# Optimization experiments

Measured on AMD Instinct MI355X. Metric: run time of the kernel, lower is better.

## Reference

```python
import jax, jax.numpy as jnp
import numpy as np

RADIUS = 50
HEADS = 4
BN_EPS = 1e-5


def setup_inputs() -> dict:
    key = jax.random.key(0)
    B, C, L = 2, 256, 1536
    D = C // HEADS
    ks = jax.random.split(key, 8)
    s = 0.05  # weight init scale
    return {
        "x": jax.random.normal(ks[0], (B, C, L), jnp.float32),
        "Wc": jax.random.normal(ks[1], (C, C), jnp.float32) * s,
        "bc": jnp.zeros((C,), jnp.float32),
        "Wq": jax.random.normal(ks[2], (C, C), jnp.float32) * s,
        "bq": jnp.zeros((C,), jnp.float32),
        "Wk": jax.random.normal(ks[3], (C, C), jnp.float32) * s,
        "bk": jnp.zeros((C,), jnp.float32),
        "emb": jax.random.normal(ks[4], (2 * RADIUS + 1, D), jnp.float32) * s,
        "Wf": jax.random.normal(ks[5], (C, C), jnp.float32) * s,
        "bf": jnp.zeros((C,), jnp.float32),
        "gamma": jnp.ones((C,), jnp.float32),
        "beta": jnp.zeros((C,), jnp.float32),
        "scale": jnp.full((C,), 0.1, jnp.float32),
    }


def reference(x, Wc, bc, Wq, bq, Wk, bk, emb, Wf, bf, gamma, beta, scale):
    B, C, L = x.shape
    H = HEADS
    D = C // H
    R = RADIUS

    def conv1x1(W, b, y):  # 1x1 Conv1d == per-position matmul
        return jnp.einsum('oc,bcl->bol', W, y) + b[None, :, None]

    def split(y):  # [B,C,L] -> [B,H,D,L]
        return y.reshape(B, H, D, L)

    content = split(conv1x1(Wc, bc, x))
    query = split(conv1x1(Wq, bq, x))
    key_ = split(conv1x1(Wk, bk, x))

    steps = jnp.arange(L)
    relative = steps[:, None] - steps[None, :]                 # [L,L]
    rel_clamped = jnp.clip(relative, -R, R)
    embs = emb[R + rel_clamped]                                # [L,L,D] gather

    dots = jnp.einsum('bhct,bhcs->bhts', query, key_)          # [B,H,L,L]
    dots = dots + 0.3 * jnp.einsum('bhct,tsc->bhts', query, embs)
    dots = jnp.where(jnp.abs(relative) <= R, dots, -jnp.inf)   # band mask

    weights = jax.nn.softmax(dots, axis=-1)                    # [B,H,L,L]

    out = jnp.einsum('bhts,bhcs->bhct', weights, content)      # [B,H,D,L]
    out = out + 0.3 * jnp.einsum('bhts,tsc->bhct', weights, embs)
    out = out.reshape(B, C, L)

    out = conv1x1(Wf, bf, out)
    # BatchNorm1d in training mode: batch stats over (B, L) per channel
    mean = out.mean(axis=(0, 2), keepdims=True)
    var = out.var(axis=(0, 2), keepdims=True)
    out = (out - mean) / jnp.sqrt(var + BN_EPS)
    out = out * gamma[None, :, None] + beta[None, :, None]
    return jax.nn.relu(out) * scale[None, :, None]
```

## Files before the change

kernel.cpp:

```cpp
#include <hip/hip_runtime.h>

typedef unsigned short u16;
typedef unsigned int u32;
typedef __bf16 bf16x8 __attribute__((ext_vector_type(8)));
typedef float f32x4 __attribute__((ext_vector_type(4)));

#define MFMA16 __builtin_amdgcn_mfma_f32_16x16x32_bf16

__device__ __forceinline__ u16 f2bf(float f) {
    u32 u = __float_as_uint(f);
    u32 r = (u + 0x7fffu + ((u >> 16) & 1u)) >> 16;
    return (u16)r;
}
__device__ __forceinline__ float bf2f(u16 h) {
    return __uint_as_float(((u32)h) << 16);
}
__device__ __forceinline__ bf16x8 ld8(const u16* p) {
    return *reinterpret_cast<const bf16x8*>(p);
}

__global__ __launch_bounds__(256) void prep(
    const float* __restrict__ x,
    const float* __restrict__ Wc, const float* __restrict__ Wq,
    const float* __restrict__ Wk, const float* __restrict__ Wf,
    const float* __restrict__ emb,
    u16* __restrict__ xT,
    u16* __restrict__ wcb, u16* __restrict__ wqb, u16* __restrict__ wkb,
    u16* __restrict__ wfb, u16* __restrict__ embR, u16* __restrict__ embT)
{
    const int tid = threadIdx.x;
    const int z = blockIdx.z;
    if (z < 2) {
        __shared__ u16 tile[64][65];
        const int b = z, c0 = blockIdx.y * 64, l0 = blockIdx.x * 64;
        const int cc = tid >> 2, lq = (tid & 3) * 16;
        const float* xp = x + (size_t)((b * 256 + c0 + cc) * 1536 + l0 + lq);
        #pragma unroll
        for (int i = 0; i < 4; ++i) {
            float4 v = *reinterpret_cast<const float4*>(xp + i * 4);
            tile[cc][lq + i * 4 + 0] = f2bf(v.x);
            tile[cc][lq + i * 4 + 1] = f2bf(v.y);
            tile[cc][lq + i * 4 + 2] = f2bf(v.z);
            tile[cc][lq + i * 4 + 3] = f2bf(v.w);
        }
        __syncthreads();
        const int ll = tid >> 2, cq = (tid & 3) * 16;
        u16* op = xT + (size_t)((b * 1536 + l0 + ll) * 256 + c0 + cq);
        #pragma unroll
        for (int i = 0; i < 16; ++i) op[i] = tile[cq + i][ll];
    } else {
        const int idx0 = (blockIdx.y * 24 + blockIdx.x) * 256 + tid;
        for (int i = idx0; i < 65536; i += 24576) {
            wcb[i] = f2bf(Wc[i]); wqb[i] = f2bf(Wq[i]);
            wkb[i] = f2bf(Wk[i]); wfb[i] = f2bf(Wf[i]);
        }
        if (idx0 < 112 * 64) {
            const int j = idx0 >> 6, d = idx0 & 63;
            embR[idx0] = (j < 101) ? f2bf(0.3f * emb[(100 - j) * 64 + d]) : (u16)0;
        }
        if (idx0 < 64 * 128) {
            const int d = idx0 >> 7, j = idx0 & 127;
            embT[idx0] = (j < 101) ? f2bf(0.3f * emb[(100 - j) * 64 + d]) : (u16)0;
        }
    }
}

__global__ __launch_bounds__(128) void gemm_qkc(
    const u16* __restrict__ xT,
    const u16* __restrict__ Wq, const float* __restrict__ bq,
    const u16* __restrict__ Wk, const float* __restrict__ bk,
    const u16* __restrict__ Wc, const float* __restrict__ bc,
    u16* __restrict__ qo, u16* __restrict__ ko, u16* __restrict__ co)
{
    const int tid = threadIdx.x, wv = tid >> 6, lane = tid & 63;
    const int l15 = lane & 15, kg8 = (lane >> 4) * 8;
    const int z = blockIdx.z, b = z & 1, which = z >> 1;
    const u16* W = (which == 0) ? Wq : (which == 1) ? Wk : Wc;
    const float* bias = (which == 0) ? bq : (which == 1) ? bk : bc;
    const int l0 = blockIdx.x * 64 + wv * 32;
    const int ch0 = blockIdx.y * 32;
    const u16* xp = xT + (size_t)(b * 1536 + l0 + l15) * 256 + kg8;
    const u16* wp = W + (size_t)(ch0 + l15) * 256 + kg8;
    const u16* ap = (which == 2) ? wp : xp;
    const u16* bp = (which == 2) ? xp : wp;

    bf16x8 a0r[8], a1r[8], b0r[8], b1r[8];
    #pragma unroll
    for (int kd = 0; kd < 8; ++kd) {
        a0r[kd] = ld8(ap + kd * 32);
        a1r[kd] = ld8(ap + 4096 + kd * 32);
        b0r[kd] = ld8(bp + kd * 32);
        b1r[kd] = ld8(bp + 4096 + kd * 32);
    }
    const f32x4 zf = {0.f, 0.f, 0.f, 0.f};
    f32x4 acc[2][2] = {{zf, zf}, {zf, zf}};
    #pragma unroll
    for (int kd = 0; kd < 8; ++kd) {
        acc[0][0] = MFMA16(a0r[kd], b0r[kd], acc[0][0], 0, 0, 0);
        acc[0][1] = MFMA16(a0r[kd], b1r[kd], acc[0][1], 0, 0, 0);
        acc[1][0] = MFMA16(a1r[kd], b0r[kd], acc[1][0], 0, 0, 0);
        acc[1][1] = MFMA16(a1r[kd], b1r[kd], acc[1][1], 0, 0, 0);
    }
    if (which < 2) {
        u16* outp = which ? ko : qo;
        float bv[2];
        bv[0] = bias[ch0 + l15];
        bv[1] = bias[ch0 + 16 + l15];
        #pragma unroll
        for (int mf = 0; mf < 2; ++mf)
            #pragma unroll
            for (int nf = 0; nf < 2; ++nf)
                #pragma unroll
                for (int r = 0; r < 4; ++r) {
                    const int row = l0 + mf * 16 + (lane >> 4) * 4 + r;
                    outp[(size_t)(b * 1536 + row) * 256 + ch0 + nf * 16 + l15] =
                        f2bf(acc[mf][nf][r] + bv[nf]);
                }
    } else {
        #pragma unroll
        for (int mf = 0; mf < 2; ++mf)
            #pragma unroll
            for (int r = 0; r < 4; ++r) {
                const int ch = ch0 + mf * 16 + (lane >> 4) * 4 + r;
                const float bv = bias[ch];
                #pragma unroll
                for (int nf = 0; nf < 2; ++nf)
                    co[(size_t)(b * 256 + ch) * 1536 + l0 + nf * 16 + l15] =
                        f2bf(acc[mf][nf][r] + bv);
            }
    }
}

__global__ __launch_bounds__(128) void gemm_f(
    const u16* __restrict__ W, const float* __restrict__ bias,
    const u16* __restrict__ srcT, u16* __restrict__ outp)
{
    const int tid = threadIdx.x, wv = tid >> 6, lane = tid & 63;
    const int l15 = lane & 15, kg8 = (lane >> 4) * 8;
    const int b = blockIdx.z;
    const int l0 = blockIdx.x * 64 + wv * 32;
    const int ch0 = blockIdx.y * 32;
    const u16* ap = W + (size_t)(ch0 + l15) * 256 + kg8;
    const u16* bp = srcT + (size_t)(b * 1536 + l0 + l15) * 256 + kg8;

    bf16x8 a0r[8], a1r[8], b0r[8], b1r[8];
    #pragma unroll
    for (int kd = 0; kd < 8; ++kd) {
        a0r[kd] = ld8(ap + kd * 32);
        a1r[kd] = ld8(ap + 4096 + kd * 32);
        b0r[kd] = ld8(bp + kd * 32);
        b1r[kd] = ld8(bp + 4096 + kd * 32);
    }
    const f32x4 zf = {0.f, 0.f, 0.f, 0.f};
    f32x4 acc[2][2] = {{zf, zf}, {zf, zf}};
    #pragma unroll
    for (int kd = 0; kd < 8; ++kd) {
        acc[0][0] = MFMA16(a0r[kd], b0r[kd], acc[0][0], 0, 0, 0);
        acc[0][1] = MFMA16(a0r[kd], b1r[kd], acc[0][1], 0, 0, 0);
        acc[1][0] = MFMA16(a1r[kd], b0r[kd], acc[1][0], 0, 0, 0);
        acc[1][1] = MFMA16(a1r[kd], b1r[kd], acc[1][1], 0, 0, 0);
    }
    #pragma unroll
    for (int mf = 0; mf < 2; ++mf)
        #pragma unroll
        for (int r = 0; r < 4; ++r) {
            const int ch = ch0 + mf * 16 + (lane >> 4) * 4 + r;
            const float bv = bias[ch];
            #pragma unroll
            for (int nf = 0; nf < 2; ++nf)
                outp[(size_t)(b * 256 + ch) * 1536 + l0 + nf * 16 + l15] =
                    f2bf(acc[mf][nf][r] + bv);
        }
}

#define WST 168
#define WBST 136
#define BST 114

__global__ __launch_bounds__(128) void attn_mfma(
    const u16* __restrict__ q, const u16* __restrict__ k,
    const u16* __restrict__ cont, const u16* __restrict__ embR,
    const u16* __restrict__ embT, u16* __restrict__ outp)
{
    __shared__ u16 wls[2][16][WST];
    __shared__ u16 wbs[2][16][WBST];
    __shared__ u16 bss[2][16][BST];
    const int tid = threadIdx.x;
    const int wv = tid >> 6, lane = tid & 63;
    const int l15 = lane & 15, kg8 = (lane >> 4) * 8;
    const int tt0 = (blockIdx.x * 2 + wv) * 16;
    const int bh = blockIdx.y, b = bh >> 2, h = bh & 3;
    u16* wl = &wls[wv][0][0];
    u16* wb = &wbs[wv][0][0];
    u16* bs = &bss[wv][0][0];

    const u16* qp = q + (size_t)(b * 1536 + tt0 + l15) * 256 + h * 64 + kg8;
    const bf16x8 a0 = ld8(qp);
    const bf16x8 a1 = ld8(qp + 32);
    bf16x8 k0r[9], k1r[9];
    #pragma unroll
    for (int nf = 0; nf < 9; ++nf) {
        int s = tt0 - 64 + nf * 16 + l15;
        int sc = s < 0 ? 0 : (s > 1535 ? 1535 : s);
        const u16* kp = k + (size_t)(b * 1536 + sc) * 256 + h * 64 + kg8;
        k0r[nf] = ld8(kp);
        k1r[nf] = ld8(kp + 32);
    }

    for (int i = lane; i < 16 * 8; i += 64) {
        const int t = i >> 3, c = 144 + ((i & 7) << 1);
        *reinterpret_cast<u32*>(&wl[t * WST + c]) = 0;
    }
    for (int i = lane; i < 16 * 27; i += 64) {
        const int t = i / 27, j = 101 + (i - t * 27);
        wb[t * WBST + j] = 0;
    }

    const f32x4 zf = {0.f, 0.f, 0.f, 0.f};
    f32x4 dacc[9];
    f32x4 eacc[7];
    #pragma unroll
    for (int i = 0; i < 9; ++i) dacc[i] = zf;
    #pragma unroll
    for (int i = 0; i < 7; ++i) eacc[i] = zf;

    #pragma unroll
    for (int nf = 0; nf < 9; ++nf) {
        dacc[nf] = MFMA16(a0, k0r[nf], dacc[nf], 0, 0, 0);
        dacc[nf] = MFMA16(a1, k1r[nf], dacc[nf], 0, 0, 0);
    }
    #pragma unroll
    for (int jf = 0; jf < 7; ++jf) {
        const u16* ep = embR + (jf * 16 + l15) * 64 + kg8;
        eacc[jf] = MFMA16(a0, ld8(ep), eacc[jf], 0, 0, 0);
        eacc[jf] = MFMA16(a1, ld8(ep + 32), eacc[jf], 0, 0, 0);
    }
    #pragma unroll
    for (int jf = 0; jf < 7; ++jf)
        #pragma unroll
        for (int r = 0; r < 4; ++r) {
            const int t = (lane >> 4) * 4 + r;
            bs[t * BST + jf * 16 + l15] = f2bf(eacc[jf][r]);
        }
    #pragma unroll
    for (int nf = 0; nf < 9; ++nf)
        #pragma unroll
        for (int r = 0; r < 4; ++r) {
            const int t = (lane >> 4) * 4 + r;
            const int cs = nf * 16 + l15;
            const int j = cs - t - 14;
            const int s = tt0 - 64 + cs;
            float v = dacc[nf][r];
            if (j >= 0 && j < 101 && s >= 0 && s < 1536)
                v += bf2f(bs[t * BST + j]);
            else
                v = -1e30f;
            dacc[nf][r] = v;
        }
    float inv[4];
    #pragma unroll
    for (int r = 0; r < 4; ++r) {
        float m = dacc[0][r];
        #pragma unroll
        for (int nf = 1; nf < 9; ++nf) m = fmaxf(m, dacc[nf][r]);
        m = fmaxf(m, __shfl_xor(m, 1));
        m = fmaxf(m, __shfl_xor(m, 2));
        m = fmaxf(m, __shfl_xor(m, 4));
        m = fmaxf(m, __shfl_xor(m, 8));
        float ss = 0.f;
        #pragma unroll
        for (int nf = 0; nf < 9; ++nf) {
            float e = __expf(dacc[nf][r] - m);
            dacc[nf][r] = e;
            ss += e;
        }
        ss += __shfl_xor(ss, 1);
        ss += __shfl_xor(ss, 2);
        ss += __shfl_xor(ss, 4);
        ss += __shfl_xor(ss, 8);
        inv[r] = 1.f / ss;
    }
    #pragma unroll
    for (int nf = 0; nf < 9; ++nf)
        #pragma unroll
        for (int r = 0; r < 4; ++r) {
            const int t = (lane >> 4) * 4 + r;
            const int cs = nf * 16 + l15;
            const u16 w16 = f2bf(dacc[nf][r] * inv[r]);
            wl[t * WST + cs] = w16;
            const int j = cs - t - 14;
            if (j >= 0 && j < 101) wb[t * WBST + j] = w16;
        }

    f32x4 oacc[4];
    #pragma unroll
    for (int i = 0; i < 4; ++i) oacc[i] = zf;
    #pragma unroll
    for (int kf = 0; kf < 5; ++kf) {
        const bf16x8 aw = ld8(&wl[l15 * WST + kf * 32 + kg8]);
        int sb = tt0 - 64 + kf * 32 + kg8;
        int sbc = sb < 0 ? 0 : (sb > 1528 ? 1528 : sb);
        #pragma unroll
        for (int nf = 0; nf < 4; ++nf) {
            const u16* cp = cont + (size_t)(b * 256 + h * 64 + nf * 16 + l15) * 1536 + sbc;
            oacc[nf] = MFMA16(aw, ld8(cp), oacc[nf], 0, 0, 0);
        }
    }
    #pragma unroll
    for (int kf = 0; kf < 4; ++kf) {
        const bf16x8 ab = ld8(&wb[l15 * WBST + kf * 32 + kg8]);
        #pragma unroll
        for (int nf = 0; nf < 4; ++nf) {
            const u16* ep = embT + (nf * 16 + l15) * 128 + kf * 32 + kg8;
            oacc[nf] = MFMA16(ab, ld8(ep), oacc[nf], 0, 0, 0);
        }
    }
    #pragma unroll
    for (int nf = 0; nf < 4; ++nf)
        #pragma unroll
        for (int r = 0; r < 4; ++r) {
            const int t = (lane >> 4) * 4 + r;
            outp[(size_t)(b * 1536 + tt0 + t) * 256 + h * 64 + nf * 16 + l15] =
                f2bf(oacc[nf][r]);
        }
}

__global__ __launch_bounds__(256) void bn_apply(
    const u16* __restrict__ pre, const float* __restrict__ gamma,
    const float* __restrict__ beta, const float* __restrict__ scale,
    float* __restrict__ out)
{
    const int o = blockIdx.x;
    const int tid = threadIdx.x;
    float v[12];
    float sum = 0.f, sumsq = 0.f;
    #pragma unroll
    for (int g = 0; g < 6; ++g) {
        const int b = (g >= 3);
        const int l = (g - 3 * b) * 512 + tid * 2;
        const u32 w = *reinterpret_cast<const u32*>(&pre[(size_t)(b * 256 + o) * 1536 + l]);
        const float v0 = __uint_as_float(w << 16);
        const float v1 = __uint_as_float(w & 0xffff0000u);
        v[g * 2] = v0; v[g * 2 + 1] = v1;
        sum += v0 + v1;
        sumsq = fmaf(v0, v0, sumsq);
        sumsq = fmaf(v1, v1, sumsq);
    }
    #pragma unroll
    for (int off = 1; off < 64; off <<= 1) {
        sum += __shfl_xor(sum, off);
        sumsq += __shfl_xor(sumsq, off);
    }
    __shared__ float rs[4], rq[4];
    const int wave = tid >> 6;
    if ((tid & 63) == 0) { rs[wave] = sum; rq[wave] = sumsq; }
    __syncthreads();
    sum = rs[0] + rs[1] + rs[2] + rs[3];
    sumsq = rq[0] + rq[1] + rq[2] + rq[3];
    const float mean = sum * (1.f / 3072.f);
    const float var = sumsq * (1.f / 3072.f) - mean * mean;
    const float is = rsqrtf(var + 1e-5f);
    const float gm = gamma[o] * is;
    const float b2 = beta[o] - mean * gm;
    const float sc = scale[o];
    #pragma unroll
    for (int g = 0; g < 6; ++g) {
        const int b = (g >= 3);
        const int l = (g - 3 * b) * 512 + tid * 2;
        float2 o2;
        o2.x = fmaxf(fmaf(v[g * 2], gm, b2), 0.f) * sc;
        o2.y = fmaxf(fmaf(v[g * 2 + 1], gm, b2), 0.f) * sc;
        *reinterpret_cast<float2*>(&out[(size_t)(b * 256 + o) * 1536 + l]) = o2;
    }
}

extern "C" void kernel_launch(void* const* d_in, const int* in_sizes, int n_in,
                              void* d_out, int out_size, void* d_ws, size_t ws_size,
                              hipStream_t stream) {
    const float* x     = (const float*)d_in[0];
    const float* Wc    = (const float*)d_in[1];
    const float* bc    = (const float*)d_in[2];
    const float* Wq    = (const float*)d_in[3];
    const float* bq    = (const float*)d_in[4];
    const float* Wk    = (const float*)d_in[5];
    const float* bk    = (const float*)d_in[6];
    const float* emb   = (const float*)d_in[7];
    const float* Wf    = (const float*)d_in[8];
    const float* bf    = (const float*)d_in[9];
    const float* gamma = (const float*)d_in[10];
    const float* beta  = (const float*)d_in[11];
    const float* scale = (const float*)d_in[12];
    float* out = (float*)d_out;
    u16* ws = (u16*)d_ws;

    const size_t NLC = 786432;
    u16* xT   = ws;
    u16* qb   = ws + NLC;
    u16* kb   = ws + 2 * NLC;
    u16* cbuf = ws + 3 * NLC;
    u16* abuf = ws + 4 * NLC;
    u16* pbuf = ws + 5 * NLC;
    u16* wcb  = ws + 6 * NLC;
    u16* wqb  = wcb + 65536;
    u16* wkb  = wqb + 65536;
    u16* wfb  = wkb + 65536;
    u16* embR = wfb + 65536;
    u16* embT = embR + 112 * 64;

    prep<<<dim3(24, 4, 3), 256, 0, stream>>>(x, Wc, Wq, Wk, Wf, emb,
                                             xT, wcb, wqb, wkb, wfb, embR, embT);
    gemm_qkc<<<dim3(24, 8, 6), 128, 0, stream>>>(xT, wqb, bq, wkb, bk, wcb, bc,
                                                 qb, kb, cbuf);
    attn_mfma<<<dim3(48, 8), 128, 0, stream>>>(qb, kb, cbuf, embR, embT, abuf);
    gemm_f<<<dim3(24, 8, 2), 128, 0, stream>>>(wfb, bf, abuf, pbuf);
    bn_apply<<<256, 256, 0, stream>>>(pbuf, gamma, beta, scale, out);
}
```

Baseline: 118.0 us.

## Fuse prep kernel into consumers: in-kernel fp32→bf16 conversion and shared x tile

Removes the separate prep kernel. The QKV GEMM now loads x in fp32, converts and transposes it into shared memory, then reuses that tile for all three projections, reading weights as fp32 and converting in registers. The attention kernel builds the scaled relative-embedding fragments directly from fp32 emb, and gemm_f converts Wf on the fly. This saves one launch and the intermediate buffers. In exchange, every block repeats the weight and embedding conversions, and the transposed embedding gather in attention uses strided scalar loads.

```diff
diff --git a/kernel.cpp b/kernel.cpp
--- a/kernel.cpp
+++ b/kernel.cpp
@@ -18,159 +18,110 @@
 __device__ __forceinline__ bf16x8 ld8(const u16* p) {
     return *reinterpret_cast<const bf16x8*>(p);
 }
-
-__global__ __launch_bounds__(256) void prep(
+__device__ __forceinline__ bf16x8 ld8f(const float* p) {
+    const float4 a = *reinterpret_cast<const float4*>(p);
+    const float4 b = *reinterpret_cast<const float4*>(p + 4);
+    union { bf16x8 v; u16 s[8]; } u;
+    u.s[0] = f2bf(a.x); u.s[1] = f2bf(a.y); u.s[2] = f2bf(a.z); u.s[3] = f2bf(a.w);
+    u.s[4] = f2bf(b.x); u.s[5] = f2bf(b.y); u.s[6] = f2bf(b.z); u.s[7] = f2bf(b.w);
+    return u.v;
+}
+__device__ __forceinline__ bf16x8 ld8f03(const float* p) {
+    const float4 a = *reinterpret_cast<const float4*>(p);
+    const float4 b = *reinterpret_cast<const float4*>(p + 4);
+    union { bf16x8 v; u16 s[8]; } u;
+    u.s[0] = f2bf(0.3f * a.x); u.s[1] = f2bf(0.3f * a.y);
+    u.s[2] = f2bf(0.3f * a.z); u.s[3] = f2bf(0.3f * a.w);
+    u.s[4] = f2bf(0.3f * b.x); u.s[5] = f2bf(0.3f * b.y);
+    u.s[6] = f2bf(0.3f * b.z); u.s[7] = f2bf(0.3f * b.w);
+    return u.v;
+}
+__device__ __forceinline__ bf16x8 zero8() {
+    union { bf16x8 v; u16 s[8]; } u;
+    #pragma unroll
+    for (int e = 0; e < 8; ++e) u.s[e] = 0;
+    return u.v;
+}
+
+__global__ __launch_bounds__(256) void gemm_qkc(
     const float* __restrict__ x,
-    const float* __restrict__ Wc, const float* __restrict__ Wq,
-    const float* __restrict__ Wk, const float* __restrict__ Wf,
-    const float* __restrict__ emb,
-    u16* __restrict__ xT,
-    u16* __restrict__ wcb, u16* __restrict__ wqb, u16* __restrict__ wkb,
-    u16* __restrict__ wfb, u16* __restrict__ embR, u16* __restrict__ embT)
-{
-    const int tid = threadIdx.x;
-    const int z = blockIdx.z;
-    if (z < 2) {
-        __shared__ u16 tile[64][65];
-        const int b = z, c0 = blockIdx.y * 64, l0 = blockIdx.x * 64;
-        const int cc = tid >> 2, lq = (tid & 3) * 16;
-        const float* xp = x + (size_t)((b * 256 + c0 + cc) * 1536 + l0 + lq);
-        #pragma unroll
-        for (int i = 0; i < 4; ++i) {
-            float4 v = *reinterpret_cast<const float4*>(xp + i * 4);
-            tile[cc][lq + i * 4 + 0] = f2bf(v.x);
-            tile[cc][lq + i * 4 + 1] = f2bf(v.y);
-            tile[cc][lq + i * 4 + 2] = f2bf(v.z);
-            tile[cc][lq + i * 4 + 3] = f2bf(v.w);
-        }
-        __syncthreads();
-        const int ll = tid >> 2, cq = (tid & 3) * 16;
-        u16* op = xT + (size_t)((b * 1536 + l0 + ll) * 256 + c0 + cq);
-        #pragma unroll
-        for (int i = 0; i < 16; ++i) op[i] = tile[cq + i][ll];
-    } else {
-        const int idx0 = (blockIdx.y * 24 + blockIdx.x) * 256 + tid;
-        for (int i = idx0; i < 65536; i += 24576) {
-            wcb[i] = f2bf(Wc[i]); wqb[i] = f2bf(Wq[i]);
-            wkb[i] = f2bf(Wk[i]); wfb[i] = f2bf(Wf[i]);
-        }
-        if (idx0 < 112 * 64) {
-            const int j = idx0 >> 6, d = idx0 & 63;
-            embR[idx0] = (j < 101) ? f2bf(0.3f * emb[(100 - j) * 64 + d]) : (u16)0;
-        }
-        if (idx0 < 64 * 128) {
-            const int d = idx0 >> 7, j = idx0 & 127;
-            embT[idx0] = (j < 101) ? f2bf(0.3f * emb[(100 - j) * 64 + d]) : (u16)0;
-        }
-    }
-}
-
-__global__ __launch_bounds__(128) void gemm_qkc(
-    const u16* __restrict__ xT,
-    const u16* __restrict__ Wq, const float* __restrict__ bq,
-    const u16* __restrict__ Wk, const float* __restrict__ bk,
-    const u16* __restrict__ Wc, const float* __restrict__ bc,
+    const float* __restrict__ Wq, const float* __restrict__ bq,
+    const float* __restrict__ Wk, const float* __restrict__ bk,
+    const float* __restrict__ Wc, const float* __restrict__ bc,
     u16* __restrict__ qo, u16* __restrict__ ko, u16* __restrict__ co)
 {
+    __shared__ u16 xs[64][264];
     const int tid = threadIdx.x, wv = tid >> 6, lane = tid & 63;
     const int l15 = lane & 15, kg8 = (lane >> 4) * 8;
-    const int z = blockIdx.z, b = z & 1, which = z >> 1;
-    const u16* W = (which == 0) ? Wq : (which == 1) ? Wk : Wc;
-    const float* bias = (which == 0) ? bq : (which == 1) ? bk : bc;
-    const int l0 = blockIdx.x * 64 + wv * 32;
-    const int ch0 = blockIdx.y * 32;
-    const u16* xp = xT + (size_t)(b * 1536 + l0 + l15) * 256 + kg8;
-    const u16* wp = W + (size_t)(ch0 + l15) * 256 + kg8;
-    const u16* ap = (which == 2) ? wp : xp;
-    const u16* bp = (which == 2) ? xp : wp;
-
-    bf16x8 a0r[8], a1r[8], b0r[8], b1r[8];
+    const int l0 = blockIdx.x * 64, ch0 = blockIdx.y * 32, b = blockIdx.z;
+
+    const int cc = tid >> 2, lq = (tid & 3) * 16;
+    #pragma unroll
+    for (int it = 0; it < 4; ++it) {
+        const int c = it * 64 + cc;
+        const float* xp = x + (size_t)((b * 256 + c) * 1536 + l0 + lq);
+        #pragma unroll
+        for (int i = 0; i < 4; ++i) {
+            const float4 v = *reinterpret_cast<const float4*>(xp + i * 4);
+            xs[lq + i * 4 + 0][c] = f2bf(v.x);
+            xs[lq + i * 4 + 1][c] = f2bf(v.y);
+            xs[lq + i * 4 + 2][c] = f2bf(v.z);
+            xs[lq + i * 4 + 3][c] = f2bf(v.w);
+        }
+    }
+    __syncthreads();
+
+    const int lw = (wv & 1) * 32;
+    const int chw = ch0 + (wv >> 1) * 16;
+    const f32x4 zf = {0.f, 0.f, 0.f, 0.f};
+
+    bf16x8 xa0[8], xa1[8];
     #pragma unroll
     for (int kd = 0; kd < 8; ++kd) {
-        a0r[kd] = ld8(ap + kd * 32);
-        a1r[kd] = ld8(ap + 4096 + kd * 32);
-        b0r[kd] = ld8(bp + kd * 32);
-        b1r[kd] = ld8(bp + 4096 + kd * 32);
-    }
-    const f32x4 zf = {0.f, 0.f, 0.f, 0.f};
-    f32x4 acc[2][2] = {{zf, zf}, {zf, zf}};
-    #pragma unroll
-    for (int kd = 0; kd < 8; ++kd) {
-        acc[0][0] = MFMA16(a0r[kd], b0r[kd], acc[0][0], 0, 0, 0);
-        acc[0][1] = MFMA16(a0r[kd], b1r[kd], acc[0][1], 0, 0, 0);
-        acc[1][0] = MFMA16(a1r[kd], b0r[kd], acc[1][0], 0, 0, 0);
-        acc[1][1] = MFMA16(a1r[kd], b1r[kd], acc[1][1], 0, 0, 0);
-    }
-    if (which < 2) {
-        u16* outp = which ? ko : qo;
-        float bv[2];
-        bv[0] = bias[ch0 + l15];
-        bv[1] = bias[ch0 + 16 + l15];
-        #pragma unroll
-        for (int mf = 0; mf < 2; ++mf)
-            #pragma unroll
-            for (int nf = 0; nf < 2; ++nf)
-                #pragma unroll
-                for (int r = 0; r < 4; ++r) {
-                    const int row = l0 + mf * 16 + (lane >> 4) * 4 + r;
-                    outp[(size_t)(b * 1536 + row) * 256 + ch0 + nf * 16 + l15] =
-                        f2bf(acc[mf][nf][r] + bv[nf]);
-                }
-    } else {
-        #pragma unroll
-        for (int mf = 0; mf < 2; ++mf)
+        xa0[kd] = ld8(&xs[lw + l15][kd * 32 + kg8]);
+        xa1[kd] = ld8(&xs[lw + 16 + l15][kd * 32 + kg8]);
+    }
+
+    #pragma unroll
+    for (int which = 0; which < 3; ++which) {
+        const float* W    = (which == 0) ? Wq : (which == 1) ? Wk : Wc;
+        const float* bias = (which == 0) ? bq : (which == 1) ? bk : bc;
+        bf16x8 wf[8];
+        #pragma unroll
+        for (int kd = 0; kd < 8; ++kd)
+            wf[kd] = ld8f(W + (size_t)(chw + l15) * 256 + kd * 32 + kg8);
+
+        if (which < 2) {
+            u16* outp = which ? ko : qo;
+            f32x4 acc0 = zf, acc1 = zf;
+            #pragma unroll
+            for (int kd = 0; kd < 8; ++kd) {
+                acc0 = MFMA16(xa0[kd], wf[kd], acc0, 0, 0, 0);
+                acc1 = MFMA16(xa1[kd], wf[kd], acc1, 0, 0, 0);
+            }
+            const float bv = bias[chw + l15];
             #pragma unroll
             for (int r = 0; r < 4; ++r) {
-                const int ch = ch0 + mf * 16 + (lane >> 4) * 4 + r;
+                const int row0 = l0 + lw + (lane >> 4) * 4 + r;
+                outp[(size_t)(b * 1536 + row0) * 256 + chw + l15] = f2bf(acc0[r] + bv);
+                outp[(size_t)(b * 1536 + row0 + 16) * 256 + chw + l15] = f2bf(acc1[r] + bv);
+            }
+        } else {
+            f32x4 acc0 = zf, acc1 = zf;
+            #pragma unroll
+            for (int kd = 0; kd < 8; ++kd) {
+                acc0 = MFMA16(wf[kd], xa0[kd], acc0, 0, 0, 0);
+                acc1 = MFMA16(wf[kd], xa1[kd], acc1, 0, 0, 0);
+            }
+            #pragma unroll
+            for (int r = 0; r < 4; ++r) {
+                const int ch = chw + (lane >> 4) * 4 + r;
                 const float bv = bias[ch];
-                #pragma unroll
-                for (int nf = 0; nf < 2; ++nf)
-                    co[(size_t)(b * 256 + ch) * 1536 + l0 + nf * 16 + l15] =
-                        f2bf(acc[mf][nf][r] + bv);
+                co[(size_t)(b * 256 + ch) * 1536 + l0 + lw + l15] = f2bf(acc0[r] + bv);
+                co[(size_t)(b * 256 + ch) * 1536 + l0 + lw + 16 + l15] = f2bf(acc1[r] + bv);
             }
-    }
-}
-
-__global__ __launch_bounds__(128) void gemm_f(
-    const u16* __restrict__ W, const float* __restrict__ bias,
-    const u16* __restrict__ srcT, u16* __restrict__ outp)
-{
-    const int tid = threadIdx.x, wv = tid >> 6, lane = tid & 63;
-    const int l15 = lane & 15, kg8 = (lane >> 4) * 8;
-    const int b = blockIdx.z;
-    const int l0 = blockIdx.x * 64 + wv * 32;
-    const int ch0 = blockIdx.y * 32;
-    const u16* ap = W + (size_t)(ch0 + l15) * 256 + kg8;
-    const u16* bp = srcT + (size_t)(b * 1536 + l0 + l15) * 256 + kg8;
-
-    bf16x8 a0r[8], a1r[8], b0r[8], b1r[8];
-    #pragma unroll
-    for (int kd = 0; kd < 8; ++kd) {
-        a0r[kd] = ld8(ap + kd * 32);
-        a1r[kd] = ld8(ap + 4096 + kd * 32);
-        b0r[kd] = ld8(bp + kd * 32);
-        b1r[kd] = ld8(bp + 4096 + kd * 32);
-    }
-    const f32x4 zf = {0.f, 0.f, 0.f, 0.f};
-    f32x4 acc[2][2] = {{zf, zf}, {zf, zf}};
-    #pragma unroll
-    for (int kd = 0; kd < 8; ++kd) {
-        acc[0][0] = MFMA16(a0r[kd], b0r[kd], acc[0][0], 0, 0, 0);
-        acc[0][1] = MFMA16(a0r[kd], b1r[kd], acc[0][1], 0, 0, 0);
-        acc[1][0] = MFMA16(a1r[kd], b0r[kd], acc[1][0], 0, 0, 0);
-        acc[1][1] = MFMA16(a1r[kd], b1r[kd], acc[1][1], 0, 0, 0);
-    }
-    #pragma unroll
-    for (int mf = 0; mf < 2; ++mf)
-        #pragma unroll
-        for (int r = 0; r < 4; ++r) {
-            const int ch = ch0 + mf * 16 + (lane >> 4) * 4 + r;
-            const float bv = bias[ch];
-            #pragma unroll
-            for (int nf = 0; nf < 2; ++nf)
-                outp[(size_t)(b * 256 + ch) * 1536 + l0 + nf * 16 + l15] =
-                    f2bf(acc[mf][nf][r] + bv);
-        }
+        }
+    }
 }
 
 #define WST 168
@@ -179,8 +130,8 @@
 
 __global__ __launch_bounds__(128) void attn_mfma(
     const u16* __restrict__ q, const u16* __restrict__ k,
-    const u16* __restrict__ cont, const u16* __restrict__ embR,
-    const u16* __restrict__ embT, u16* __restrict__ outp)
+    const u16* __restrict__ cont, const float* __restrict__ emb,
+    u16* __restrict__ outp)
 {
     __shared__ u16 wls[2][16][WST];
     __shared__ u16 wbs[2][16][WBST];
@@ -231,9 +182,18 @@
     }
     #pragma unroll
     for (int jf = 0; jf < 7; ++jf) {
-        const u16* ep = embR + (jf * 16 + l15) * 64 + kg8;
-        eacc[jf] = MFMA16(a0, ld8(ep), eacc[jf], 0, 0, 0);
-        eacc[jf] = MFMA16(a1, ld8(ep + 32), eacc[jf], 0, 0, 0);
+        const int j = jf * 16 + l15;
+        bf16x8 e0, e1;
+        if (j <= 100) {
+            const float* ep = emb + (size_t)(100 - j) * 64;
+            e0 = ld8f03(ep + kg8);
+            e1 = ld8f03(ep + kg8 + 32);
+        } else {
+            e0 = zero8();
+            e1 = zero8();
+        }
+        eacc[jf] = MFMA16(a0, e0, eacc[jf], 0, 0, 0);
+        eacc[jf] = MFMA16(a1, e1, eacc[jf], 0, 0, 0);
     }
     #pragma unroll
     for (int jf = 0; jf < 7; ++jf)
@@ -311,8 +271,14 @@
         const bf16x8 ab = ld8(&wb[l15 * WBST + kf * 32 + kg8]);
         #pragma unroll
         for (int nf = 0; nf < 4; ++nf) {
-            const u16* ep = embT + (nf * 16 + l15) * 128 + kf * 32 + kg8;
-            oacc[nf] = MFMA16(ab, ld8(ep), oacc[nf], 0, 0, 0);
+            const int d = nf * 16 + l15;
+            union { bf16x8 v; u16 s[8]; } u;
+            #pragma unroll
+            for (int e = 0; e < 8; ++e) {
+                const int j = kf * 32 + kg8 + e;
+                u.s[e] = (j <= 100) ? f2bf(0.3f * emb[(size_t)(100 - j) * 64 + d]) : (u16)0;
+            }
+            oacc[nf] = MFMA16(ab, u.v, oacc[nf], 0, 0, 0);
         }
     }
     #pragma unroll
@@ -322,6 +288,47 @@
             const int t = (lane >> 4) * 4 + r;
             outp[(size_t)(b * 1536 + tt0 + t) * 256 + h * 64 + nf * 16 + l15] =
                 f2bf(oacc[nf][r]);
+        }
+}
+
+__global__ __launch_bounds__(128) void gemm_f(
+    const float* __restrict__ Wf, const float* __restrict__ bias,
+    const u16* __restrict__ srcT, u16* __restrict__ outp)
+{
+    const int tid = threadIdx.x, wv = tid >> 6, lane = tid & 63;
+    const int l15 = lane & 15, kg8 = (lane >> 4) * 8;
+    const int b = blockIdx.z;
+    const int l0 = blockIdx.x * 64 + wv * 32;
+    const int ch0 = blockIdx.y * 32;
+    const u16* bp = srcT + (size_t)(b * 1536 + l0 + l15) * 256 + kg8;
+
+    bf16x8 a0r[8], a1r[8], b0r[8], b1r[8];
+    #pragma unroll
+    for (int kd = 0; kd < 8; ++kd) {
+        a0r[kd] = ld8f(Wf + (size_t)(ch0 + l15) * 256 + kd * 32 + kg8);
+        a1r[kd] = ld8f(Wf + (size_t)(ch0 + 16 + l15) * 256 + kd * 32 + kg8);
+        b0r[kd] = ld8(bp + kd * 32);
+        b1r[kd] = ld8(bp + 4096 + kd * 32);
+    }
+    const f32x4 zf = {0.f, 0.f, 0.f, 0.f};
+    f32x4 acc[2][2] = {{zf, zf}, {zf, zf}};
+    #pragma unroll
+    for (int kd = 0; kd < 8; ++kd) {
+        acc[0][0] = MFMA16(a0r[kd], b0r[kd], acc[0][0], 0, 0, 0);
+        acc[0][1] = MFMA16(a0r[kd], b1r[kd], acc[0][1], 0, 0, 0);
+        acc[1][0] = MFMA16(a1r[kd], b0r[kd], acc[1][0], 0, 0, 0);
+        acc[1][1] = MFMA16(a1r[kd], b1r[kd], acc[1][1], 0, 0, 0);
+    }
+    #pragma unroll
+    for (int mf = 0; mf < 2; ++mf)
+        #pragma unroll
+        for (int r = 0; r < 4; ++r) {
+            const int ch = ch0 + mf * 16 + (lane >> 4) * 4 + r;
+            const float bv = bias[ch];
+            #pragma unroll
+            for (int nf = 0; nf < 2; ++nf)
+                outp[(size_t)(b * 256 + ch) * 1536 + l0 + nf * 16 + l15] =
+                    f2bf(acc[mf][nf][r] + bv);
         }
 }
 
@@ -394,24 +401,15 @@
     u16* ws = (u16*)d_ws;
 
     const size_t NLC = 786432;
-    u16* xT   = ws;
-    u16* qb   = ws + NLC;
-    u16* kb   = ws + 2 * NLC;
-    u16* cbuf = ws + 3 * NLC;
-    u16* abuf = ws + 4 * NLC;
-    u16* pbuf = ws + 5 * NLC;
-    u16* wcb  = ws + 6 * NLC;
-    u16* wqb  = wcb + 65536;
-    u16* wkb  = wqb + 65536;
-    u16* wfb  = wkb + 65536;
-    u16* embR = wfb + 65536;
-    u16* embT = embR + 112 * 64;
-
-    prep<<<dim3(24, 4, 3), 256, 0, stream>>>(x, Wc, Wq, Wk, Wf, emb,
-                                             xT, wcb, wqb, wkb, wfb, embR, embT);
-    gemm_qkc<<<dim3(24, 8, 6), 128, 0, stream>>>(xT, wqb, bq, wkb, bk, wcb, bc,
+    u16* qb   = ws;
+    u16* kb   = ws + NLC;
+    u16* cbuf = ws + 2 * NLC;
+    u16* abuf = ws + 3 * NLC;
+    u16* pbuf = ws + 4 * NLC;
+
+    gemm_qkc<<<dim3(24, 8, 2), 256, 0, stream>>>(x, Wq, bq, Wk, bk, Wc, bc,
                                                  qb, kb, cbuf);
-    attn_mfma<<<dim3(48, 8), 128, 0, stream>>>(qb, kb, cbuf, embR, embT, abuf);
-    gemm_f<<<dim3(24, 8, 2), 128, 0, stream>>>(wfb, bf, abuf, pbuf);
+    attn_mfma<<<dim3(48, 8), 128, 0, stream>>>(qb, kb, cbuf, emb, abuf);
+    gemm_f<<<dim3(24, 8, 2), 128, 0, stream>>>(Wf, bf, abuf, pbuf);
     bn_apply<<<256, 256, 0, stream>>>(pbuf, gamma, beta, scale, out);
 }
```

After: 124.6 us. +5.5%, slower.
